# Kernel tuning notes

Measured on AMD Instinct MI355X. Metric: run time of the kernel, lower is better.

## Reference

```python
import jax, jax.numpy as jnp
import numpy as np

B, S, D = 2, 2048, 1024        # batch, seq_len, d_model
E, F, K = 8, 2048, 2           # num_experts, ffn_hidden_size, moe_top_k


def setup_inputs() -> dict:
    key = jax.random.key(0)
    k0, k1, k2, k3, k4 = jax.random.split(key, 5)
    scale = 0.02
    x = jax.random.normal(k0, (B, S, D), dtype=jnp.float32)
    w1 = jax.random.normal(k1, (E * F, D), dtype=jnp.float32) * scale
    v1 = jax.random.normal(k2, (E * F, D), dtype=jnp.float32) * scale
    w2 = jax.random.normal(k3, (E * F, D), dtype=jnp.float32) * scale
    router_w = jax.random.normal(k4, (E, D), dtype=jnp.float32) * scale
    return {"x": x, "w1": w1, "v1": v1, "w2": w2, "router_w": router_w}


def reference(x, w1, v1, w2, router_w):
    # ---- Router (deterministic; no jitter) ----
    logits = jnp.einsum("bsd,ed->bse", x, router_w)              # (B,S,E)
    weights = jax.nn.softmax(logits.astype(jnp.float32), axis=-1)
    top_weights, top_experts = jax.lax.top_k(weights, K)          # (B,S,K)
    # moe_normalize_expert_weights = 1 -> L1 renormalization of top-k weights
    norm = jnp.sum(jnp.abs(top_weights), axis=-1, keepdims=True)
    top_weights = (top_weights / norm).astype(x.dtype)

    # ---- Experts: dense SwiGLU per expert, masked combine (faithful to loop) ----
    w1e = w1.reshape(E, F, D)
    v1e = v1.reshape(E, F, D)
    w2e = w2.reshape(E, F, D)
    out = jnp.zeros_like(x)
    for e in range(E):  # fixed small expert count; structurally distinct weights
        gate = jnp.sum(jnp.where(top_experts == e, top_weights, 0.0), axis=-1)  # (B,S)
        h1 = jax.nn.silu(jnp.einsum("bsd,fd->bsf", x, w1e[e]))
        h = h1 * jnp.einsum("bsd,fd->bsf", x, v1e[e])             # (B,S,F)
        y = jnp.einsum("bsf,fd->bsd", h, w2e[e])                  # (B,S,D)
        out = out + gate[..., None] * y
    return out
```

## Files before the change

### kernel.cpp

```cpp
#include <hip/hip_runtime.h>
#include <hip/hip_bf16.h>
#include <stdint.h>

#define D_MODEL 1024
#define NEXP 8
#define FF 2048
#define TOPK 2
#define NTOK 4096
#define MT 128
#define BK 64
#define MAXROWS (NTOK*TOPK + NEXP*MT)
#define MAXTILES (MAXROWS/MT)

typedef __bf16 bf16x8 __attribute__((ext_vector_type(8)));
typedef float f32x4 __attribute__((ext_vector_type(4)));

__device__ inline unsigned short f2b(float f){
  __hip_bfloat16 h = __float2bfloat16(f);
  return __builtin_bit_cast(unsigned short, h);
}

__device__ inline void gl2lds16(const unsigned short* g, unsigned short* l){
  __builtin_amdgcn_global_load_lds(
      (const __attribute__((address_space(1))) unsigned int*)g,
      (__attribute__((address_space(3))) unsigned int*)l, 16, 0, 0);
}

__global__ void zero_out_kernel(float* out, int n){
  int i = blockIdx.x*256 + threadIdx.x;
  if (i < n) out[i] = 0.f;
}

__global__ __launch_bounds__(256) void conv_kernel(
    const float* __restrict__ in, unsigned short* __restrict__ out, long n4)
{
  long i = (long)blockIdx.x*256 + threadIdx.x;
  if (i >= n4) return;
  float4 v = reinterpret_cast<const float4*>(in)[i];
  ushort4 o;
  o.x = f2b(v.x); o.y = f2b(v.y); o.z = f2b(v.z); o.w = f2b(v.w);
  reinterpret_cast<ushort4*>(out)[i] = o;
}


__global__ void init_kernel(int* perm, int* ctrl){
  int i = blockIdx.x*256 + threadIdx.x;
  if (i < MAXROWS) perm[i] = -1;
  if (i < 64) ctrl[i] = 0;
}

__global__ __launch_bounds__(256) void router_kernel(
    const float* __restrict__ x, const float* __restrict__ rw,
    float* __restrict__ topw, int* __restrict__ tope, int* __restrict__ counts)
{
  const int wid = threadIdx.x >> 6, lane = threadIdx.x & 63;
  const int t = blockIdx.x*4 + wid;
  float p[NEXP];
  #pragma unroll
  for (int e=0;e<NEXP;e++) p[e] = 0.f;
  for (int i=0;i<16;i++){
    int d = i*64 + lane;
    float xv = x[(long)t*D_MODEL + d];
    #pragma unroll
    for (int e=0;e<NEXP;e++) p[e] += xv * rw[e*D_MODEL + d];
  }
  #pragma unroll
  for (int e=0;e<NEXP;e++)
    for (int off=32; off; off>>=1) p[e] += __shfl_xor(p[e], off, 64);
  if (lane == 0){
    float mx = p[0];
    #pragma unroll
    for (int e=1;e<NEXP;e++) mx = fmaxf(mx, p[e]);
    float w[NEXP]; float s = 0.f;
    #pragma unroll
    for (int e=0;e<NEXP;e++){ w[e] = expf(p[e]-mx); s += w[e]; }
    #pragma unroll
    for (int e=0;e<NEXP;e++) w[e] /= s;
    int e1 = 0;
    #pragma unroll
    for (int e=1;e<NEXP;e++) if (w[e] > w[e1]) e1 = e;
    int e2 = -1;
    #pragma unroll
    for (int e=0;e<NEXP;e++) if (e != e1 && (e2 < 0 || w[e] > w[e2])) e2 = e;
    float s2 = w[e1] + w[e2];
    topw[t*2+0] = w[e1]/s2;
    topw[t*2+1] = w[e2]/s2;
    tope[t*2+0] = e1; tope[t*2+1] = e2;
    atomicAdd(&counts[e1], 1); atomicAdd(&counts[e2], 1);
  }
}

__global__ void partition_kernel(const int* ctrl, int* segStart, int* tileExpert){
  if (threadIdx.x == 0 && blockIdx.x == 0){
    int off = 0, tile = 0;
    for (int e=0;e<NEXP;e++){
      segStart[e] = off;
      int padded = ((ctrl[e] + MT - 1)/MT)*MT;
      off += padded;
      for (int k=0;k<padded/MT && tile < MAXTILES;k++) tileExpert[tile++] = e;
    }
    segStart[NEXP] = off;
    while (tile < MAXTILES) tileExpert[tile++] = -1;
  }
}

__global__ void scatter_kernel(const int* tope, const int* segStart, int* fill,
                               int* perm, int* rowOf){
  int i = blockIdx.x*256 + threadIdx.x;
  int e = tope[i];
  int pos = segStart[e] + atomicAdd(&fill[e], 1);
  if (pos >= 0 && pos < MAXROWS){ perm[pos] = i >> 1; rowOf[i] = pos; }
}

__global__ void transpose_w2(const float* __restrict__ w2,
                             unsigned short* __restrict__ w2t){
  __shared__ unsigned short tl[32][33];
  const int e = blockIdx.z;
  const int d0 = blockIdx.x*32, f0 = blockIdx.y*32;
  const int tx = threadIdx.x, ty = threadIdx.y;
  #pragma unroll
  for (int i=0;i<4;i++)
    tl[ty + i*8][tx] = f2b(w2[((long)(e*FF + f0 + ty + i*8))*D_MODEL + d0 + tx]);
  __syncthreads();
  #pragma unroll
  for (int i=0;i<4;i++)
    w2t[((long)e*D_MODEL + d0 + ty + i*8)*FF + f0 + tx] = tl[tx][ty + i*8];
}

__global__ __launch_bounds__(256, 3) void gemm1_swiglu(
    const unsigned short* __restrict__ x,
    const unsigned short* __restrict__ w1,
    const unsigned short* __restrict__ v1,
    const int* __restrict__ perm,
    const int* __restrict__ tileExpert,
    unsigned short* __restrict__ Hg)
{
  const int b = blockIdx.x;
  const int xcd = b & 7, s = b >> 3;
  const int mt = xcd*9 + (s % 9);
  const int nt = s / 9;
  int e = tileExpert[mt];
  if (e < 0) return;
  e &= 7;
  __shared__ alignas(16) unsigned short As [MT*BK];
  __shared__ alignas(16) unsigned short B1s[MT*BK];
  __shared__ alignas(16) unsigned short B2s[MT*BK];
  const int tid = threadIdx.x;
  const int lane = tid & 63;
  const int wr = ((tid >> 7) & 1) * 64;
  const int wc = ((tid >> 6) & 1) * 64;

  long aoff[4]; long boff[4]; int dstIdx[4];
  #pragma unroll
  for (int i=0;i<4;i++){
    int idx = tid + 256*i;
    int r = idx >> 3, c = idx & 7;
    int sc = c ^ (r & 7);
    int tok = perm[mt*MT + r]; if (tok < 0 || tok >= NTOK) tok = 0;
    aoff[i] = (long)tok * D_MODEL + sc*8;
    boff[i] = ((long)e*FF + nt*MT + r) * D_MODEL + sc*8;
    dstIdx[i] = idx * 8;
  }
  f32x4 zero = {0.f,0.f,0.f,0.f};
  f32x4 acc1[4][4], acc2[4][4];
  #pragma unroll
  for (int i=0;i<4;i++)
    #pragma unroll
    for (int j=0;j<4;j++){ acc1[i][j] = zero; acc2[i][j] = zero; }

  for (int k0 = 0; k0 < D_MODEL; k0 += BK){
    __syncthreads();
    #pragma unroll
    for (int i=0;i<4;i++) gl2lds16(x  + aoff[i] + k0, &As [dstIdx[i]]);
    #pragma unroll
    for (int i=0;i<4;i++) gl2lds16(w1 + boff[i] + k0, &B1s[dstIdx[i]]);
    #pragma unroll
    for (int i=0;i<4;i++) gl2lds16(v1 + boff[i] + k0, &B2s[dstIdx[i]]);
    __syncthreads();
    #pragma unroll
    for (int kk = 0; kk < BK; kk += 32){
      const int q = (lane >> 4) + (kk >> 3);
      bf16x8 a[4], bb1[4], bb2[4];
      #pragma unroll
      for (int i=0;i<4;i++){
        int r = wr + i*16 + (lane & 15);
        a[i] = *reinterpret_cast<const bf16x8*>(&As[r*BK + ((q ^ (r&7))*8)]);
      }
      #pragma unroll
      for (int j=0;j<4;j++){
        int n = wc + j*16 + (lane & 15);
        int adr = n*BK + ((q ^ (n&7))*8);
        bb1[j] = *reinterpret_cast<const bf16x8*>(&B1s[adr]);
        bb2[j] = *reinterpret_cast<const bf16x8*>(&B2s[adr]);
      }
      #pragma unroll
      for (int i=0;i<4;i++)
        #pragma unroll
        for (int j=0;j<4;j++){
          acc1[i][j] = __builtin_amdgcn_mfma_f32_16x16x32_bf16(a[i], bb1[j], acc1[i][j], 0,0,0);
          acc2[i][j] = __builtin_amdgcn_mfma_f32_16x16x32_bf16(a[i], bb2[j], acc2[i][j], 0,0,0);
        }
    }
  }
  const int mrow0 = mt*MT + wr + ((lane >> 4) << 2);
  const int ncol0 = nt*MT + wc + (lane & 15);
  #pragma unroll
  for (int i=0;i<4;i++)
    #pragma unroll
    for (int j=0;j<4;j++)
      #pragma unroll
      for (int rr=0;rr<4;rr++){
        float g = acc1[i][j][rr];
        float u = acc2[i][j][rr];
        float h = (g / (1.0f + __expf(-g))) * u;
        Hg[(long)(mrow0 + i*16 + rr)*FF + (ncol0 + j*16)] = f2b(h);
      }
}

__global__ __launch_bounds__(256, 3) void gemm2_kernel(
    const unsigned short* __restrict__ Hg,
    const unsigned short* __restrict__ w2t,
    const int* __restrict__ tileExpert,
    float* __restrict__ Yg)
{
  const int b = blockIdx.x;
  const int xcd = b & 7, s = b >> 3;
  const int mt = xcd + 8*(s >> 3);
  const int nt = s & 7;
  int e = tileExpert[mt];
  if (e < 0) return;
  e &= 7;
  __shared__ alignas(16) unsigned short As[MT*BK];
  __shared__ alignas(16) unsigned short Bs[MT*BK];
  const int tid = threadIdx.x;
  const int lane = tid & 63;
  const int wr = ((tid >> 7) & 1) * 64;
  const int wc = ((tid >> 6) & 1) * 64;

  long aoff[4]; long boff[4]; int dstIdx[4];
  #pragma unroll
  for (int i=0;i<4;i++){
    int idx = tid + 256*i;
    int r = idx >> 3, c = idx & 7;
    int sc = c ^ (r & 7);
    aoff[i] = (long)(mt*MT + r) * FF + sc*8;
    boff[i] = ((long)e*D_MODEL + nt*MT + r) * FF + sc*8;
    dstIdx[i] = idx * 8;
  }
  f32x4 zero = {0.f,0.f,0.f,0.f};
  f32x4 acc[4][4];
  #pragma unroll
  for (int i=0;i<4;i++)
    #pragma unroll
    for (int j=0;j<4;j++) acc[i][j] = zero;

  for (int k0 = 0; k0 < FF; k0 += BK){
    __syncthreads();
    #pragma unroll
    for (int i=0;i<4;i++) gl2lds16(Hg  + aoff[i] + k0, &As[dstIdx[i]]);
    #pragma unroll
    for (int i=0;i<4;i++) gl2lds16(w2t + boff[i] + k0, &Bs[dstIdx[i]]);
    __syncthreads();
    #pragma unroll
    for (int kk = 0; kk < BK; kk += 32){
      const int q = (lane >> 4) + (kk >> 3);
      bf16x8 a[4], bb[4];
      #pragma unroll
      for (int i=0;i<4;i++){
        int r = wr + i*16 + (lane & 15);
        a[i] = *reinterpret_cast<const bf16x8*>(&As[r*BK + ((q ^ (r&7))*8)]);
      }
      #pragma unroll
      for (int j=0;j<4;j++){
        int n = wc + j*16 + (lane & 15);
        bb[j] = *reinterpret_cast<const bf16x8*>(&Bs[n*BK + ((q ^ (n&7))*8)]);
      }
      #pragma unroll
      for (int i=0;i<4;i++)
        #pragma unroll
        for (int j=0;j<4;j++)
          acc[i][j] = __builtin_amdgcn_mfma_f32_16x16x32_bf16(a[i], bb[j], acc[i][j], 0,0,0);
    }
  }
  const int mrow0 = mt*MT + wr + ((lane >> 4) << 2);
  const int ncol0 = nt*MT + wc + (lane & 15);
  #pragma unroll
  for (int i=0;i<4;i++)
    #pragma unroll
    for (int j=0;j<4;j++)
      #pragma unroll
      for (int rr=0;rr<4;rr++)
        Yg[(long)(mrow0 + i*16 + rr)*D_MODEL + (ncol0 + j*16)] = acc[i][j][rr];
}

__global__ __launch_bounds__(256) void combine_kernel(
    const float* __restrict__ Yg, const float* __restrict__ topw,
    const int* __restrict__ rowOf, float* __restrict__ out)
{
  const int t = blockIdx.x;
  const int d = threadIdx.x * 4;
  const float wA = topw[2*t], wB = topw[2*t+1];
  long rA = rowOf[2*t], rB = rowOf[2*t+1];
  if (rA < 0 || rA >= MAXROWS) rA = 0;
  if (rB < 0 || rB >= MAXROWS) rB = 0;
  float4 a = *reinterpret_cast<const float4*>(Yg + rA*D_MODEL + d);
  float4 b = *reinterpret_cast<const float4*>(Yg + rB*D_MODEL + d);
  float4 o;
  o.x = wA*a.x + wB*b.x;
  o.y = wA*a.y + wB*b.y;
  o.z = wA*a.z + wB*b.z;
  o.w = wA*a.w + wB*b.w;
  *reinterpret_cast<float4*>(out + (long)t*D_MODEL + d) = o;
}

extern "C" void kernel_launch(void* const* d_in, const int* in_sizes, int n_in,
                              void* d_out, int out_size, void* d_ws, size_t ws_size,
                              hipStream_t stream)
{
  const float* x  = (const float*)d_in[0];
  const float* w1 = (const float*)d_in[1];
  const float* v1 = (const float*)d_in[2];
  const float* w2 = (const float*)d_in[3];
  const float* rw = (const float*)d_in[4];
  float* out = (float*)d_out;
  (void)in_sizes; (void)n_in;

  size_t need = 0;
  auto count = [&](size_t b){ size_t r = need; need += (b + 255) & ~(size_t)255; return r; };
  size_t o_topw = count((size_t)NTOK*TOPK*sizeof(float));
  size_t o_tope = count((size_t)NTOK*TOPK*sizeof(int));
  size_t o_ctrl = count(64*sizeof(int));
  size_t o_seg  = count(16*sizeof(int));
  size_t o_te   = count(MAXTILES*sizeof(int));
  size_t o_perm = count(MAXROWS*sizeof(int));
  size_t o_rowOf= count((size_t)NTOK*TOPK*sizeof(int));
  size_t o_xb   = count((size_t)NTOK*D_MODEL*2);
  size_t o_w1b  = count((size_t)NEXP*FF*D_MODEL*2);
  size_t o_v1b  = count((size_t)NEXP*FF*D_MODEL*2);
  size_t o_w2t  = count((size_t)NEXP*D_MODEL*FF*2);
  size_t o_Hg   = count((size_t)MAXROWS*FF*2);
  size_t o_Yg   = count((size_t)MAXROWS*D_MODEL*sizeof(float));

  if (ws_size < need){
    zero_out_kernel<<<(out_size+255)/256, 256, 0, stream>>>(out, out_size);
    return;
  }

  char* base = (char*)d_ws;
  float* topw      = (float*)(base + o_topw);
  int*   tope      = (int*)  (base + o_tope);
  int*   ctrl      = (int*)  (base + o_ctrl);
  int*   segStart  = (int*)  (base + o_seg);
  int*   tileExpert= (int*)  (base + o_te);
  int*   perm      = (int*)  (base + o_perm);
  int*   rowOf     = (int*)  (base + o_rowOf);
  unsigned short* xb  = (unsigned short*)(base + o_xb);
  unsigned short* w1b = (unsigned short*)(base + o_w1b);
  unsigned short* v1b = (unsigned short*)(base + o_v1b);
  unsigned short* w2t = (unsigned short*)(base + o_w2t);
  unsigned short* Hg  = (unsigned short*)(base + o_Hg);
  float*          Yg  = (float*)         (base + o_Yg);

  const long nx4 = (long)NTOK*D_MODEL/4;
  const long nw4 = (long)NEXP*FF*D_MODEL/4;

  init_kernel     <<<(MAXROWS+255)/256, 256, 0, stream>>>(perm, ctrl);
  router_kernel   <<<NTOK/4, 256, 0, stream>>>(x, rw, topw, tope, ctrl);
  partition_kernel<<<1, 64, 0, stream>>>(ctrl, segStart, tileExpert);
  scatter_kernel  <<<NTOK*TOPK/256, 256, 0, stream>>>(tope, segStart, ctrl+8, perm, rowOf);
  conv_kernel     <<<(nx4+255)/256, 256, 0, stream>>>(x,  xb,  nx4);
  conv_kernel     <<<(nw4+255)/256, 256, 0, stream>>>(w1, w1b, nw4);
  conv_kernel     <<<(nw4+255)/256, 256, 0, stream>>>(v1, v1b, nw4);
  transpose_w2    <<<dim3(D_MODEL/32, FF/32, NEXP), dim3(32,8), 0, stream>>>(w2, w2t);
  gemm1_swiglu    <<<MAXTILES*(FF/MT), 256, 0, stream>>>(xb, w1b, v1b, perm, tileExpert, Hg);
  gemm2_kernel    <<<MAXTILES*(D_MODEL/MT), 256, 0, stream>>>(Hg, w2t, tileExpert, Yg);
  combine_kernel  <<<NTOK, 256, 0, stream>>>(Yg, topw, rowOf, out);
}
```

Before: 628.6 us.

## Double-buffer LDS tiles with async prefetch in both expert GEMMs

```diff
diff --git a/kernel.cpp b/kernel.cpp
--- a/kernel.cpp
+++ b/kernel.cpp
@@ -8,7 +8,7 @@
 #define TOPK 2
 #define NTOK 4096
 #define MT 128
-#define BK 64
+#define KSTEP 32
 #define MAXROWS (NTOK*TOPK + NEXP*MT)
 #define MAXTILES (MAXROWS/MT)
 
@@ -127,7 +127,7 @@
     w2t[((long)e*D_MODEL + d0 + ty + i*8)*FF + f0 + tx] = tl[tx][ty + i*8];
 }
 
-__global__ __launch_bounds__(256, 3) void gemm1_swiglu(
+__global__ __launch_bounds__(256, 2) void gemm1_swiglu(
     const unsigned short* __restrict__ x,
     const unsigned short* __restrict__ w1,
     const unsigned short* __restrict__ v1,
@@ -142,20 +142,20 @@
   int e = tileExpert[mt];
   if (e < 0) return;
   e &= 7;
-  __shared__ alignas(16) unsigned short As [MT*BK];
-  __shared__ alignas(16) unsigned short B1s[MT*BK];
-  __shared__ alignas(16) unsigned short B2s[MT*BK];
+  __shared__ alignas(16) unsigned short As [2][MT*KSTEP];
+  __shared__ alignas(16) unsigned short B1s[2][MT*KSTEP];
+  __shared__ alignas(16) unsigned short B2s[2][MT*KSTEP];
   const int tid = threadIdx.x;
   const int lane = tid & 63;
   const int wr = ((tid >> 7) & 1) * 64;
   const int wc = ((tid >> 6) & 1) * 64;
 
-  long aoff[4]; long boff[4]; int dstIdx[4];
-  #pragma unroll
-  for (int i=0;i<4;i++){
+  long aoff[2]; long boff[2]; int dstIdx[2];
+  #pragma unroll
+  for (int i=0;i<2;i++){
     int idx = tid + 256*i;
-    int r = idx >> 3, c = idx & 7;
-    int sc = c ^ (r & 7);
+    int r = idx >> 2, c = idx & 3;
+    int sc = c ^ ((r >> 1) & 3);
     int tok = perm[mt*MT + r]; if (tok < 0 || tok >= NTOK) tok = 0;
     aoff[i] = (long)tok * D_MODEL + sc*8;
     boff[i] = ((long)e*FF + nt*MT + r) * D_MODEL + sc*8;
@@ -168,39 +168,56 @@
     #pragma unroll
     for (int j=0;j<4;j++){ acc1[i][j] = zero; acc2[i][j] = zero; }
 
-  for (int k0 = 0; k0 < D_MODEL; k0 += BK){
-    __syncthreads();
-    #pragma unroll
-    for (int i=0;i<4;i++) gl2lds16(x  + aoff[i] + k0, &As [dstIdx[i]]);
-    #pragma unroll
-    for (int i=0;i<4;i++) gl2lds16(w1 + boff[i] + k0, &B1s[dstIdx[i]]);
-    #pragma unroll
-    for (int i=0;i<4;i++) gl2lds16(v1 + boff[i] + k0, &B2s[dstIdx[i]]);
-    __syncthreads();
-    #pragma unroll
-    for (int kk = 0; kk < BK; kk += 32){
-      const int q = (lane >> 4) + (kk >> 3);
-      bf16x8 a[4], bb1[4], bb2[4];
-      #pragma unroll
-      for (int i=0;i<4;i++){
-        int r = wr + i*16 + (lane & 15);
-        a[i] = *reinterpret_cast<const bf16x8*>(&As[r*BK + ((q ^ (r&7))*8)]);
+  #pragma unroll
+  for (int i=0;i<2;i++) gl2lds16(x  + aoff[i], &As [0][dstIdx[i]]);
+  #pragma unroll
+  for (int i=0;i<2;i++) gl2lds16(w1 + boff[i], &B1s[0][dstIdx[i]]);
+  #pragma unroll
+  for (int i=0;i<2;i++) gl2lds16(v1 + boff[i], &B2s[0][dstIdx[i]]);
+
+  const int NK = D_MODEL / KSTEP;
+  #pragma unroll 2
+  for (int t=0; t<NK; ++t){
+    const int cur = t & 1;
+    if (t+1 < NK){
+      const int k0 = (t+1)*KSTEP;
+      #pragma unroll
+      for (int i=0;i<2;i++) gl2lds16(x  + aoff[i] + k0, &As [cur^1][dstIdx[i]]);
+      #pragma unroll
+      for (int i=0;i<2;i++) gl2lds16(w1 + boff[i] + k0, &B1s[cur^1][dstIdx[i]]);
+      #pragma unroll
+      for (int i=0;i<2;i++) gl2lds16(v1 + boff[i] + k0, &B2s[cur^1][dstIdx[i]]);
+      asm volatile("s_waitcnt vmcnt(6)" ::: "memory");
+    } else {
+      asm volatile("s_waitcnt vmcnt(0)" ::: "memory");
+    }
+    __builtin_amdgcn_s_barrier();
+    asm volatile("" ::: "memory");
+
+    const int q = lane >> 4;
+    bf16x8 a[4], bb1[4], bb2[4];
+    #pragma unroll
+    for (int i=0;i<4;i++){
+      int r = wr + i*16 + (lane & 15);
+      a[i] = *reinterpret_cast<const bf16x8*>(&As[cur][r*KSTEP + ((q ^ ((r>>1)&3))*8)]);
+    }
+    #pragma unroll
+    for (int j=0;j<4;j++){
+      int n = wc + j*16 + (lane & 15);
+      int adr = n*KSTEP + ((q ^ ((n>>1)&3))*8);
+      bb1[j] = *reinterpret_cast<const bf16x8*>(&B1s[cur][adr]);
+      bb2[j] = *reinterpret_cast<const bf16x8*>(&B2s[cur][adr]);
+    }
+    #pragma unroll
+    for (int i=0;i<4;i++)
+      #pragma unroll
+      for (int j=0;j<4;j++){
+        acc1[i][j] = __builtin_amdgcn_mfma_f32_16x16x32_bf16(a[i], bb1[j], acc1[i][j], 0,0,0);
+        acc2[i][j] = __builtin_amdgcn_mfma_f32_16x16x32_bf16(a[i], bb2[j], acc2[i][j], 0,0,0);
       }
-      #pragma unroll
-      for (int j=0;j<4;j++){
-        int n = wc + j*16 + (lane & 15);
-        int adr = n*BK + ((q ^ (n&7))*8);
-        bb1[j] = *reinterpret_cast<const bf16x8*>(&B1s[adr]);
-        bb2[j] = *reinterpret_cast<const bf16x8*>(&B2s[adr]);
-      }
-      #pragma unroll
-      for (int i=0;i<4;i++)
-        #pragma unroll
-        for (int j=0;j<4;j++){
-          acc1[i][j] = __builtin_amdgcn_mfma_f32_16x16x32_bf16(a[i], bb1[j], acc1[i][j], 0,0,0);
-          acc2[i][j] = __builtin_amdgcn_mfma_f32_16x16x32_bf16(a[i], bb2[j], acc2[i][j], 0,0,0);
-        }
-    }
+    asm volatile("s_waitcnt lgkmcnt(0)" ::: "memory");
+    __builtin_amdgcn_s_barrier();
+    asm volatile("" ::: "memory");
   }
   const int mrow0 = mt*MT + wr + ((lane >> 4) << 2);
   const int ncol0 = nt*MT + wc + (lane & 15);
@@ -230,19 +247,19 @@
   int e = tileExpert[mt];
   if (e < 0) return;
   e &= 7;
-  __shared__ alignas(16) unsigned short As[MT*BK];
-  __shared__ alignas(16) unsigned short Bs[MT*BK];
+  __shared__ alignas(16) unsigned short As[2][MT*KSTEP];
+  __shared__ alignas(16) unsigned short Bs[2][MT*KSTEP];
   const int tid = threadIdx.x;
   const int lane = tid & 63;
   const int wr = ((tid >> 7) & 1) * 64;
   const int wc = ((tid >> 6) & 1) * 64;
 
-  long aoff[4]; long boff[4]; int dstIdx[4];
-  #pragma unroll
-  for (int i=0;i<4;i++){
+  long aoff[2]; long boff[2]; int dstIdx[2];
+  #pragma unroll
+  for (int i=0;i<2;i++){
     int idx = tid + 256*i;
-    int r = idx >> 3, c = idx & 7;
-    int sc = c ^ (r & 7);
+    int r = idx >> 2, c = idx & 3;
+    int sc = c ^ ((r >> 1) & 3);
     aoff[i] = (long)(mt*MT + r) * FF + sc*8;
     boff[i] = ((long)e*D_MODEL + nt*MT + r) * FF + sc*8;
     dstIdx[i] = idx * 8;
@@ -254,33 +271,49 @@
     #pragma unroll
     for (int j=0;j<4;j++) acc[i][j] = zero;
 
-  for (int k0 = 0; k0 < FF; k0 += BK){
-    __syncthreads();
-    #pragma unroll
-    for (int i=0;i<4;i++) gl2lds16(Hg  + aoff[i] + k0, &As[dstIdx[i]]);
-    #pragma unroll
-    for (int i=0;i<4;i++) gl2lds16(w2t + boff[i] + k0, &Bs[dstIdx[i]]);
-    __syncthreads();
-    #pragma unroll
-    for (int kk = 0; kk < BK; kk += 32){
-      const int q = (lane >> 4) + (kk >> 3);
-      bf16x8 a[4], bb[4];
-      #pragma unroll
-      for (int i=0;i<4;i++){
-        int r = wr + i*16 + (lane & 15);
-        a[i] = *reinterpret_cast<const bf16x8*>(&As[r*BK + ((q ^ (r&7))*8)]);
-      }
-      #pragma unroll
-      for (int j=0;j<4;j++){
-        int n = wc + j*16 + (lane & 15);
-        bb[j] = *reinterpret_cast<const bf16x8*>(&Bs[n*BK + ((q ^ (n&7))*8)]);
-      }
-      #pragma unroll
-      for (int i=0;i<4;i++)
-        #pragma unroll
-        for (int j=0;j<4;j++)
-          acc[i][j] = __builtin_amdgcn_mfma_f32_16x16x32_bf16(a[i], bb[j], acc[i][j], 0,0,0);
-    }
+  #pragma unroll
+  for (int i=0;i<2;i++) gl2lds16(Hg  + aoff[i], &As[0][dstIdx[i]]);
+  #pragma unroll
+  for (int i=0;i<2;i++) gl2lds16(w2t + boff[i], &Bs[0][dstIdx[i]]);
+
+  const int NK = FF / KSTEP;
+  #pragma unroll 2
+  for (int t=0; t<NK; ++t){
+    const int cur = t & 1;
+    if (t+1 < NK){
+      const int k0 = (t+1)*KSTEP;
+      #pragma unroll
+      for (int i=0;i<2;i++) gl2lds16(Hg  + aoff[i] + k0, &As[cur^1][dstIdx[i]]);
+      #pragma unroll
+      for (int i=0;i<2;i++) gl2lds16(w2t + boff[i] + k0, &Bs[cur^1][dstIdx[i]]);
+      asm volatile("s_waitcnt vmcnt(4)" ::: "memory");
+    } else {
+      asm volatile("s_waitcnt vmcnt(0)" ::: "memory");
+    }
+    __builtin_amdgcn_s_barrier();
+    asm volatile("" ::: "memory");
+
+    const int q = lane >> 4;
+    bf16x8 a[4], bb[4];
+    #pragma unroll
+    for (int i=0;i<4;i++){
+      int r = wr + i*16 + (lane & 15);
+      a[i] = *reinterpret_cast<const bf16x8*>(&As[cur][r*KSTEP + ((q ^ ((r>>1)&3))*8)]);
+    }
+    #pragma unroll
+    for (int j=0;j<4;j++){
+      int n = wc + j*16 + (lane & 15);
+      bb[j] = *reinterpret_cast<const bf16x8*>(&Bs[cur][n*KSTEP + ((q ^ ((n>>1)&3))*8)]);
+    }
+    #pragma unroll
+    for (int i=0;i<4;i++)
+      #pragma unroll
+      for (int j=0;j<4;j++)
+        acc[i][j] = __builtin_amdgcn_mfma_f32_16x16x32_bf16(a[i], bb[j], acc[i][j], 0,0,0);
+
+    asm volatile("s_waitcnt lgkmcnt(0)" ::: "memory");
+    __builtin_amdgcn_s_barrier();
+    asm volatile("" ::: "memory");
   }
   const int mrow0 = mt*MT + wr + ((lane >> 4) << 2);
   const int ncol0 = nt*MT + wc + (lane & 15);
```

After: 534.8 us. 1.18x faster.
